# Performance work log

Hardware: AMD Instinct MI355X
Metric: run time of the kernel (lower is better)

The kernel has to match this reference:

```python
import jax, jax.numpy as jnp
import numpy as np

CUTOFF = 5.0
COULOMB_CONSTANT = 14.3996454784936  # eV * Angstrom / e^2
SQRT2 = 1.4142135623730951
N_NODES = 500000
N_EDGES = 16000000


def polynomial_cutoff(r, cutoff):
    ratio = r / cutoff
    f = 1.0 - 6.0 * ratio**5 + 15.0 * ratio**4 - 10.0 * ratio**3
    return jnp.where(r <= cutoff, f, 0.0)


def setup_inputs() -> dict:
    key = jax.random.key(0)
    k1, k2, k3, k4, k5 = jax.random.split(key, 5)
    charge = jax.random.normal(k1, (N_NODES,), dtype=jnp.float32)
    # sigma in (0.5, 1.5): positive Gaussian widths
    sigma = jax.random.uniform(k2, (N_NODES,), dtype=jnp.float32) + 0.5
    # bond_dist in (0.1, CUTOFF)
    bond_dist = jax.random.uniform(k3, (N_EDGES,), dtype=jnp.float32) * (CUTOFF - 0.1) + 0.1
    src = jax.random.randint(k4, (N_EDGES,), 0, N_NODES, dtype=jnp.int32)
    dst = jax.random.randint(k5, (N_EDGES,), 0, N_NODES, dtype=jnp.int32)
    return {"charge": charge, "sigma": sigma, "bond_dist": bond_dist, "src": src, "dst": dst}


def reference(charge, sigma, bond_dist, src, dst):
    # Edge-wise message: q_dst * erf(r / (sqrt2 * gamma)) * fcut(r) / r * K
    gamma = jnp.sqrt(sigma[src] ** 2 + sigma[dst] ** 2)  # [E]
    msg = (
        charge[dst]
        * jax.scipy.special.erf(bond_dist / (SQRT2 * gamma))
        * polynomial_cutoff(bond_dist, CUTOFF)
        / bond_dist
    ) * COULOMB_CONSTANT
    # Sum-aggregate messages at destination nodes (DGL fn.sum semantics)
    elec_pot = jax.ops.segment_sum(msg, dst, num_segments=charge.shape[0])
    return elec_pot
```

## Files before the change

### kernel.cpp

```cpp
#include <hip/hip_runtime.h>
#include <hip/hip_fp16.h>
#include <math.h>
#include <stdint.h>

#define CUTOFF_F     5.0f
#define INV_CUTOFF   0.2f
#define KCOUL        14.3996454784936f
#define INV_SQRT2    0.7071067811865475f

typedef int            vint4    __attribute__((ext_vector_type(4)));
typedef float          vfloat4  __attribute__((ext_vector_type(4)));
typedef uint32_t       vuint4   __attribute__((ext_vector_type(4)));
typedef unsigned short vushort8 __attribute__((ext_vector_type(8)));

#define WSHIFT        12
#define WINDOW        4096
#define NB            123
#define WGS_PER_B     8
#define NWG2          (NB * WGS_PER_B)
#define EPT           8
#define EPB           4096
#define OFFS_STRIDE   128
#define SPAN_MAX      512

__device__ __forceinline__ float erf_approx(float x) {
    const float a1 = 0.254829592f, a2 = -0.284496736f, a3 = 1.421413741f,
                a4 = -1.453152027f, a5 = 1.061405429f, p = 0.3275911f;
    float t = __builtin_amdgcn_rcpf(fmaf(p, x, 1.0f));
    float poly = t * fmaf(t, fmaf(t, fmaf(t, fmaf(t, a5, a4), a3), a2), a1);
    return 1.0f - poly * __expf(-x * x);
}

__device__ __forceinline__ float edge_val(float rr, float s2sum) {
    float inv_gamma = rsqrtf(s2sum);
    float x  = rr * INV_CUTOFF;
    float fc = fmaf(x * x * x, fmaf(x, fmaf(-6.0f, x, 15.0f), -10.0f), 1.0f);
    fc = (rr <= CUTOFF_F) ? fc : 0.0f;
    return erf_approx(rr * INV_SQRT2 * inv_gamma) * fc * KCOUL
         * __builtin_amdgcn_rcpf(rr);
}

__global__ __launch_bounds__(256, 6) void p1_bin(
    const float* __restrict__ bond,
    const int*   __restrict__ src,
    const int*   __restrict__ dst,
    unsigned short* __restrict__ offs,
    uint32_t*       __restrict__ sl_out,
    unsigned short* __restrict__ r_out,
    int n_edges)
{
    __shared__ uint32_t hist[NB];
    __shared__ uint32_t scan_s[NB + 1];
    __shared__ alignas(16) uint32_t       buf_sl[EPB];
    __shared__ alignas(16) unsigned short buf_r[EPB];

    const int tid = threadIdx.x;
    const int e0  = blockIdx.x * EPB;

    if (tid < NB) hist[tid] = 0;
    __syncthreads();

    int   dA[EPT], sA[EPT], dB[EPT], sB[EPT];
    float rA[EPT], rB[EPT];
    const bool full = (e0 + EPB <= n_edges);
    if (full) {
        const vint4*   dp = (const vint4*)(dst + e0) + tid;
        const vint4*   sp = (const vint4*)(src + e0) + tid;
        const vfloat4* rp = (const vfloat4*)(bond + e0) + tid;
        vint4 d0 = __builtin_nontemporal_load(dp);
        vint4 d1 = __builtin_nontemporal_load(dp + 256);
        vint4 s0 = __builtin_nontemporal_load(sp);
        vint4 s1 = __builtin_nontemporal_load(sp + 256);
        vfloat4 r0 = __builtin_nontemporal_load(rp);
        vfloat4 r1 = __builtin_nontemporal_load(rp + 256);
        vint4 d2 = __builtin_nontemporal_load(dp + 512);
        vint4 d3 = __builtin_nontemporal_load(dp + 768);
        vint4 s2 = __builtin_nontemporal_load(sp + 512);
        vint4 s3 = __builtin_nontemporal_load(sp + 768);
        vfloat4 r2 = __builtin_nontemporal_load(rp + 512);
        vfloat4 r3 = __builtin_nontemporal_load(rp + 768);
        dA[0]=d0.x; dA[1]=d0.y; dA[2]=d0.z; dA[3]=d0.w;
        dA[4]=d1.x; dA[5]=d1.y; dA[6]=d1.z; dA[7]=d1.w;
        sA[0]=s0.x; sA[1]=s0.y; sA[2]=s0.z; sA[3]=s0.w;
        sA[4]=s1.x; sA[5]=s1.y; sA[6]=s1.z; sA[7]=s1.w;
        rA[0]=r0.x; rA[1]=r0.y; rA[2]=r0.z; rA[3]=r0.w;
        rA[4]=r1.x; rA[5]=r1.y; rA[6]=r1.z; rA[7]=r1.w;
        dB[0]=d2.x; dB[1]=d2.y; dB[2]=d2.z; dB[3]=d2.w;
        dB[4]=d3.x; dB[5]=d3.y; dB[6]=d3.z; dB[7]=d3.w;
        sB[0]=s2.x; sB[1]=s2.y; sB[2]=s2.z; sB[3]=s2.w;
        sB[4]=s3.x; sB[5]=s3.y; sB[6]=s3.z; sB[7]=s3.w;
        rB[0]=r2.x; rB[1]=r2.y; rB[2]=r2.z; rB[3]=r2.w;
        rB[4]=r3.x; rB[5]=r3.y; rB[6]=r3.z; rB[7]=r3.w;
    } else {
        #pragma unroll
        for (int j = 0; j < EPT; ++j) {
            int eA = e0 + (j >> 2) * 1024 + tid * 4 + (j & 3);
            int eB = eA + 2048;
            if (eA < n_edges) { dA[j] = dst[eA]; sA[j] = src[eA]; rA[j] = bond[eA]; }
            else dA[j] = -1;
            if (eB < n_edges) { dB[j] = dst[eB]; sB[j] = src[eB]; rB[j] = bond[eB]; }
            else dB[j] = -1;
        }
    }

    uint32_t slA[EPT], brA[EPT], slB[EPT], brB[EPT];
    unsigned short hrA[EPT], hrB[EPT];
    #pragma unroll
    for (int j = 0; j < EPT; ++j) {
        if (dA[j] >= 0) {
            unsigned b = (unsigned)dA[j] >> WSHIFT;
            uint32_t r = atomicAdd(&hist[b], 1u);
            brA[j] = (b << 16) | r;
            slA[j] = ((uint32_t)sA[j] << WSHIFT) | ((unsigned)dA[j] & (WINDOW - 1));
            hrA[j] = __half_as_ushort(__float2half_rn(rA[j]));
        } else brA[j] = 0xFFFFFFFFu;
    }
    #pragma unroll
    for (int j = 0; j < EPT; ++j) {
        if (dB[j] >= 0) {
            unsigned b = (unsigned)dB[j] >> WSHIFT;
            uint32_t r = atomicAdd(&hist[b], 1u);
            brB[j] = (b << 16) | r;
            slB[j] = ((uint32_t)sB[j] << WSHIFT) | ((unsigned)dB[j] & (WINDOW - 1));
            hrB[j] = __half_as_ushort(__float2half_rn(rB[j]));
        } else brB[j] = 0xFFFFFFFFu;
    }
    __syncthreads();

    if (tid < 64) {
        int i0 = 2 * tid, i1 = 2 * tid + 1;
        uint32_t v0 = (i0 < NB) ? hist[i0] : 0u;
        uint32_t v1 = (i1 < NB) ? hist[i1] : 0u;
        uint32_t s  = v0 + v1;
        uint32_t inc = s;
        #pragma unroll
        for (int d = 1; d < 64; d <<= 1) {
            uint32_t up = __shfl_up(inc, d, 64);
            if (tid >= d) inc += up;
        }
        uint32_t excl = inc - s;
        if (i0 < NB) scan_s[i0] = excl;
        if (i1 < NB) scan_s[i1] = excl + v0;
        if (tid == 63) scan_s[NB] = inc;
    }
    __syncthreads();

    #pragma unroll
    for (int j = 0; j < EPT; ++j)
        if (brA[j] != 0xFFFFFFFFu) {
            uint32_t p = scan_s[brA[j] >> 16] + (brA[j] & 0xFFFFu);
            buf_sl[p] = slA[j]; buf_r[p] = hrA[j];
        }
    #pragma unroll
    for (int j = 0; j < EPT; ++j)
        if (brB[j] != 0xFFFFFFFFu) {
            uint32_t p = scan_s[brB[j] >> 16] + (brB[j] & 0xFFFFu);
            buf_sl[p] = slB[j]; buf_r[p] = hrB[j];
        }
    __syncthreads();

    if (tid <= NB)
        offs[(size_t)blockIdx.x * OFFS_STRIDE + tid] = (unsigned short)scan_s[tid];

    {
        const vuint4* bs = (const vuint4*)buf_sl;
        vuint4* os = (vuint4*)(sl_out + (size_t)blockIdx.x * EPB);
        #pragma unroll
        for (int i = 0; i < EPB / 4 / 256; ++i)
            __builtin_nontemporal_store(bs[tid + i * 256], os + tid + i * 256);
        const vushort8* br = (const vushort8*)buf_r;
        vushort8* orr = (vushort8*)(r_out + (size_t)blockIdx.x * EPB);
        #pragma unroll
        for (int i = 0; i < EPB / 8 / 256; ++i)
            __builtin_nontemporal_store(br[tid + i * 256], orr + tid + i * 256);
    }
}

__global__ __launch_bounds__(256) void p2_acc(
    const uint32_t*       __restrict__ sl_in,
    const unsigned short* __restrict__ r_in,
    const unsigned short* __restrict__ offs,
    const float*          __restrict__ sigma,
    float*                __restrict__ partials,
    int n_nodes, int nblk)
{
    __shared__ float acc[WINDOW];
    __shared__ float sig[WINDOW];
    __shared__ unsigned short offLo[SPAN_MAX];
    __shared__ unsigned short offHi[SPAN_MAX];

    const int g = blockIdx.x;
    const int b = g / WGS_PER_B;
    const int w = g % WGS_PER_B;

    vfloat4* accv = (vfloat4*)acc;
    for (int i = threadIdx.x; i < WINDOW / 4; i += 256)
        accv[i] = (vfloat4){0.f, 0.f, 0.f, 0.f};

    const int nbase  = b << WSHIFT;
    const int nvalid = (n_nodes - nbase < WINDOW) ? (n_nodes - nbase) : WINDOW;
    if (nvalid == WINDOW) {
        vfloat4* sv = (vfloat4*)sig;
        const vfloat4* gp = (const vfloat4*)(sigma + nbase);
        for (int i = threadIdx.x; i < WINDOW / 4; i += 256) sv[i] = gp[i];
    } else {
        for (int i = threadIdx.x; i < WINDOW; i += 256)
            sig[i] = (i < nvalid) ? sigma[nbase + i] : 0.f;
    }

    const int span = (nblk + WGS_PER_B - 1) / WGS_PER_B;
    const int blk0 = w * span;
    int blkN = nblk - blk0;
    if (blkN > span) blkN = span;
    if (blkN < 0) blkN = 0;
    for (int i = threadIdx.x; i < blkN; i += 256) {
        size_t o = (size_t)(blk0 + i) * OFFS_STRIDE + b;
        offLo[i] = offs[o];
        offHi[i] = offs[o + 1];
    }
    __syncthreads();

    const int wave = threadIdx.x >> 6, lane = threadIdx.x & 63;
    for (int i = wave; i < blkN; i += 4) {
        uint32_t lo  = offLo[i];
        uint32_t len = (uint32_t)offHi[i] - lo;
        const uint32_t*       slb = sl_in + (size_t)(blk0 + i) * EPB + lo;
        const unsigned short* rb  = r_in  + (size_t)(blk0 + i) * EPB + lo;
        for (uint32_t k = lane; k < len; k += 64) {
            uint32_t sl = slb[k];
            float rr = __half2float(__ushort_as_half(rb[k]));
            float ss = sigma[sl >> WSHIFT];
            float sd = sig[sl & (WINDOW - 1)];
            float v  = edge_val(rr, fmaf(ss, ss, sd * sd));
            atomicAdd(&acc[sl & (WINDOW - 1)], v);
        }
    }
    __syncthreads();

    vfloat4* outp = (vfloat4*)(partials + (size_t)g * WINDOW);
    for (int i = threadIdx.x; i < WINDOW / 4; i += 256)
        __builtin_nontemporal_store(accv[i], outp + i);
}

__global__ __launch_bounds__(256) void p3_reduce(
    const float* __restrict__ partials,
    const float* __restrict__ charge,
    float*       __restrict__ out, int n_nodes)
{
    int n = blockIdx.x * 256 + threadIdx.x;
    if (n >= n_nodes) return;
    unsigned b     = (unsigned)n >> WSHIFT;
    unsigned local = (unsigned)n & (WINDOW - 1);
    const float* p = partials + ((size_t)b * WGS_PER_B) * WINDOW + local;
    float sum = 0.0f;
    #pragma unroll
    for (int w = 0; w < WGS_PER_B; ++w)
        sum += __builtin_nontemporal_load(p + (size_t)w * WINDOW);
    out[n] = charge[n] * sum;
}

__global__ __launch_bounds__(256) void edge_msg_atomic(
    const float* __restrict__ charge, const float* __restrict__ sigma,
    const float* __restrict__ bond, const int* __restrict__ src,
    const int* __restrict__ dst, float* __restrict__ out, int n_edges)
{
    int i = blockIdx.x * blockDim.x + threadIdx.x;
    if (i < n_edges) {
        float ss = sigma[src[i]], sd = sigma[dst[i]];
        float msg = charge[dst[i]] * edge_val(bond[i], fmaf(ss, ss, sd * sd));
        atomicAdd(&out[dst[i]], msg);
    }
}

extern "C" void kernel_launch(void* const* d_in, const int* in_sizes, int n_in,
                              void* d_out, int out_size, void* d_ws, size_t ws_size,
                              hipStream_t stream) {
    const float* charge = (const float*)d_in[0];
    const float* sigma  = (const float*)d_in[1];
    const float* bond   = (const float*)d_in[2];
    const int*   src    = (const int*)d_in[3];
    const int*   dst    = (const int*)d_in[4];
    float* out = (float*)d_out;

    int n_nodes = in_sizes[0];
    int n_edges = in_sizes[2];

    int nblk = (n_edges + EPB - 1) / EPB;
    int span = (nblk + WGS_PER_B - 1) / WGS_PER_B;

    size_t offs_b = (size_t)nblk * OFFS_STRIDE * sizeof(unsigned short);
    size_t sl_b   = (size_t)nblk * EPB * sizeof(uint32_t);
    size_t r_b    = (size_t)nblk * EPB * sizeof(unsigned short);
    size_t part_b = (size_t)NWG2 * WINDOW * sizeof(float);
    size_t need   = offs_b + sl_b + r_b + part_b;

    if (n_nodes <= NB * WINDOW && need <= ws_size && span <= SPAN_MAX) {
        unsigned short* offs = (unsigned short*)d_ws;
        uint32_t*       slp  = (uint32_t*)((char*)d_ws + offs_b);
        unsigned short* rp   = (unsigned short*)((char*)d_ws + offs_b + sl_b);
        float* partial = (float*)((char*)d_ws + offs_b + sl_b + r_b);

        p1_bin<<<nblk, 256, 0, stream>>>(bond, src, dst, offs, slp, rp, n_edges);
        p2_acc<<<NWG2, 256, 0, stream>>>(slp, rp, offs, sigma, partial,
                                         n_nodes, nblk);
        int blocks3 = (n_nodes + 255) / 256;
        p3_reduce<<<blocks3, 256, 0, stream>>>(partial, charge, out, n_nodes);
    } else {
        (void)hipMemsetAsync(out, 0, (size_t)n_nodes * sizeof(float), stream);
        int blocks = (n_edges + 255) / 256;
        edge_msg_atomic<<<blocks, 256, 0, stream>>>(charge, sigma, bond, src, dst,
                                                    out, n_edges);
    }
}
```

Before: 346.2 us.

## Flatten per-block segments via prefix scan for balanced wave work in p2_acc

Replaces the per-source-block wave loop, where each wave processed one short segment with partially idle lanes, with a flattened edge index space. A wave-level scan builds cumulative segment lengths, each wave takes an equal contiguous chunk, and lanes locate their segment by binary search plus a linear walk. The intent is to remove lane underutilization on short segments (about 4096/123 ≈ 33 edges each) and to balance load across waves. The cost is an extra scan, a barrier and per-lane segment walks. A launch-bounds occupancy hint is also added.

```diff
diff --git a/kernel.cpp b/kernel.cpp
--- a/kernel.cpp
+++ b/kernel.cpp
@@ -176,7 +176,7 @@
     }
 }
 
-__global__ __launch_bounds__(256) void p2_acc(
+__global__ __launch_bounds__(256, 4) void p2_acc(
     const uint32_t*       __restrict__ sl_in,
     const unsigned short* __restrict__ r_in,
     const unsigned short* __restrict__ offs,
@@ -187,7 +187,7 @@
     __shared__ float acc[WINDOW];
     __shared__ float sig[WINDOW];
     __shared__ unsigned short offLo[SPAN_MAX];
-    __shared__ unsigned short offHi[SPAN_MAX];
+    __shared__ uint32_t cum[SPAN_MAX + 1];
 
     const int g = blockIdx.x;
     const int b = g / WGS_PER_B;
@@ -215,24 +215,61 @@
     if (blkN < 0) blkN = 0;
     for (int i = threadIdx.x; i < blkN; i += 256) {
         size_t o = (size_t)(blk0 + i) * OFFS_STRIDE + b;
-        offLo[i] = offs[o];
-        offHi[i] = offs[o + 1];
+        unsigned short lo = offs[o];
+        offLo[i] = lo;
+        cum[i] = (uint32_t)offs[o + 1] - lo;
+    }
+    __syncthreads();
+
+    if (threadIdx.x < 64) {
+        const int base = threadIdx.x * 8;
+        uint32_t v[8]; uint32_t s = 0;
+        #pragma unroll
+        for (int j = 0; j < 8; ++j) { v[j] = (base + j < blkN) ? cum[base + j] : 0u; s += v[j]; }
+        uint32_t inc = s;
+        #pragma unroll
+        for (int d = 1; d < 64; d <<= 1) {
+            uint32_t up = __shfl_up(inc, d, 64);
+            if (threadIdx.x >= d) inc += up;
+        }
+        uint32_t excl = inc - s;
+        #pragma unroll
+        for (int j = 0; j < 8; ++j) { uint32_t t = v[j]; cum[base + j] = excl; excl += t; }
+        if (threadIdx.x == 63) cum[SPAN_MAX] = inc;
     }
     __syncthreads();
 
     const int wave = threadIdx.x >> 6, lane = threadIdx.x & 63;
-    for (int i = wave; i < blkN; i += 4) {
-        uint32_t lo  = offLo[i];
-        uint32_t len = (uint32_t)offHi[i] - lo;
-        const uint32_t*       slb = sl_in + (size_t)(blk0 + i) * EPB + lo;
-        const unsigned short* rb  = r_in  + (size_t)(blk0 + i) * EPB + lo;
-        for (uint32_t k = lane; k < len; k += 64) {
-            uint32_t sl = slb[k];
-            float rr = __half2float(__ushort_as_half(rb[k]));
-            float ss = sigma[sl >> WSHIFT];
-            float sd = sig[sl & (WINDOW - 1)];
-            float v  = edge_val(rr, fmaf(ss, ss, sd * sd));
-            atomicAdd(&acc[sl & (WINDOW - 1)], v);
+    const uint32_t T = cum[blkN];
+
+    const uint32_t chunk = (T + 3) >> 2;
+    const uint32_t f0    = (uint32_t)wave * chunk;
+    uint32_t fend        = f0 + chunk;
+    if (fend > T) fend = T;
+
+    if (f0 < fend) {
+        int l = 0, r = blkN;
+        while (l < r) {
+            int m = (l + r) >> 1;
+            if (cum[m + 1] <= f0) l = m + 1; else r = m;
+        }
+        int i = l;
+
+        for (uint32_t fb = f0; fb < fend; fb += 64) {
+            uint32_t f = fb + lane;
+            int ii = i;
+            if (f < fend) {
+                while (cum[ii + 1] <= f) ++ii;
+                uint32_t k = f - cum[ii];
+                size_t addr = (size_t)(blk0 + ii) * EPB + offLo[ii] + k;
+                uint32_t sl = sl_in[addr];
+                float rr = __half2float(__ushort_as_half(r_in[addr]));
+                float ss = sigma[sl >> WSHIFT];
+                float sd = sig[sl & (WINDOW - 1)];
+                float v  = edge_val(rr, fmaf(ss, ss, sd * sd));
+                atomicAdd(&acc[sl & (WINDOW - 1)], v);
+            }
+            i = __shfl(ii, 63);
         }
     }
     __syncthreads();
```

Result: no change. 345.4 us (-0.2%).

## Bin edges into global per-window buckets via atomic reservation and halve window size

Applied to the files above, without the earlier changes.

The binning pass now reserves space in per-destination-window global buckets (fixed capacity CAP) with an atomic counter per bucket. It scatters each block's sorted edges directly into those buckets, so the accumulation pass reads one contiguous, vector-loadable range per window instead of walking per-block offset tables. The window shrinks to 2048 nodes with 245 buckets, and occupancy hints are retuned. The catch is that the binning writes become narrow scattered stores, and there is no per-bucket overflow check, so a skewed destination distribution that exceeds CAP in one bucket would corrupt results.

```diff
diff --git a/kernel.cpp b/kernel.cpp
--- a/kernel.cpp
+++ b/kernel.cpp
@@ -11,17 +11,16 @@
 typedef int            vint4    __attribute__((ext_vector_type(4)));
 typedef float          vfloat4  __attribute__((ext_vector_type(4)));
 typedef uint32_t       vuint4   __attribute__((ext_vector_type(4)));
-typedef unsigned short vushort8 __attribute__((ext_vector_type(8)));
-
-#define WSHIFT        12
-#define WINDOW        4096
-#define NB            123
+typedef unsigned short vushort4 __attribute__((ext_vector_type(4)));
+
+#define WSHIFT        11
+#define WINDOW        2048
+#define NB            245
 #define WGS_PER_B     8
 #define NWG2          (NB * WGS_PER_B)
 #define EPT           8
 #define EPB           4096
-#define OFFS_STRIDE   128
-#define SPAN_MAX      512
+#define CAP           71680
 
 __device__ __forceinline__ float erf_approx(float x) {
     const float a1 = 0.254829592f, a2 = -0.284496736f, a3 = 1.421413741f,
@@ -40,19 +39,21 @@
          * __builtin_amdgcn_rcpf(rr);
 }
 
-__global__ __launch_bounds__(256, 6) void p1_bin(
+__global__ __launch_bounds__(256, 4) void p1_bin(
     const float* __restrict__ bond,
     const int*   __restrict__ src,
     const int*   __restrict__ dst,
-    unsigned short* __restrict__ offs,
+    uint32_t*       __restrict__ ctr,
     uint32_t*       __restrict__ sl_out,
     unsigned short* __restrict__ r_out,
     int n_edges)
 {
     __shared__ uint32_t hist[NB];
     __shared__ uint32_t scan_s[NB + 1];
+    __shared__ uint32_t gbase[NB];
     __shared__ alignas(16) uint32_t       buf_sl[EPB];
     __shared__ alignas(16) unsigned short buf_r[EPB];
+    __shared__ uint8_t  bkt[EPB];
 
     const int tid = threadIdx.x;
     const int e0  = blockIdx.x * EPB;
@@ -128,10 +129,10 @@
     __syncthreads();
 
     if (tid < 64) {
-        int i0 = 2 * tid, i1 = 2 * tid + 1;
-        uint32_t v0 = (i0 < NB) ? hist[i0] : 0u;
-        uint32_t v1 = (i1 < NB) ? hist[i1] : 0u;
-        uint32_t s  = v0 + v1;
+        const int base = tid * 4;
+        uint32_t v[4]; uint32_t s = 0;
+        #pragma unroll
+        for (int j = 0; j < 4; ++j) { v[j] = (base + j < NB) ? hist[base + j] : 0u; s += v[j]; }
         uint32_t inc = s;
         #pragma unroll
         for (int d = 1; d < 64; d <<= 1) {
@@ -139,9 +140,11 @@
             if (tid >= d) inc += up;
         }
         uint32_t excl = inc - s;
-        if (i0 < NB) scan_s[i0] = excl;
-        if (i1 < NB) scan_s[i1] = excl + v0;
-        if (tid == 63) scan_s[NB] = inc;
+        #pragma unroll
+        for (int j = 0; j < 4; ++j) {
+            if (base + j <= NB) scan_s[base + j] = excl;
+            excl += v[j];
+        }
     }
     __syncthreads();
 
@@ -149,45 +152,45 @@
     for (int j = 0; j < EPT; ++j)
         if (brA[j] != 0xFFFFFFFFu) {
             uint32_t p = scan_s[brA[j] >> 16] + (brA[j] & 0xFFFFu);
-            buf_sl[p] = slA[j]; buf_r[p] = hrA[j];
+            buf_sl[p] = slA[j]; buf_r[p] = hrA[j]; bkt[p] = (uint8_t)(brA[j] >> 16);
         }
     #pragma unroll
     for (int j = 0; j < EPT; ++j)
         if (brB[j] != 0xFFFFFFFFu) {
             uint32_t p = scan_s[brB[j] >> 16] + (brB[j] & 0xFFFFu);
-            buf_sl[p] = slB[j]; buf_r[p] = hrB[j];
-        }
-    __syncthreads();
-
-    if (tid <= NB)
-        offs[(size_t)blockIdx.x * OFFS_STRIDE + tid] = (unsigned short)scan_s[tid];
-
-    {
-        const vuint4* bs = (const vuint4*)buf_sl;
-        vuint4* os = (vuint4*)(sl_out + (size_t)blockIdx.x * EPB);
-        #pragma unroll
-        for (int i = 0; i < EPB / 4 / 256; ++i)
-            __builtin_nontemporal_store(bs[tid + i * 256], os + tid + i * 256);
-        const vushort8* br = (const vushort8*)buf_r;
-        vushort8* orr = (vushort8*)(r_out + (size_t)blockIdx.x * EPB);
-        #pragma unroll
-        for (int i = 0; i < EPB / 8 / 256; ++i)
-            __builtin_nontemporal_store(br[tid + i * 256], orr + tid + i * 256);
-    }
-}
-
-__global__ __launch_bounds__(256) void p2_acc(
+            buf_sl[p] = slB[j]; buf_r[p] = hrB[j]; bkt[p] = (uint8_t)(brB[j] >> 16);
+        }
+
+    if (tid < NB) {
+        uint32_t len = scan_s[tid + 1] - scan_s[tid];
+        uint32_t base = atomicAdd(&ctr[tid], len);
+        gbase[tid] = (uint32_t)tid * CAP + base - scan_s[tid];
+    }
+    __syncthreads();
+
+    const int total = (int)scan_s[NB];
+    #pragma unroll
+    for (int i = 0; i < EPB / 256; ++i) {
+        int p = tid + i * 256;
+        if (p < total) {
+            unsigned bb = bkt[p];
+            uint32_t addr = gbase[bb] + (uint32_t)p;
+            __builtin_nontemporal_store(buf_sl[p], sl_out + addr);
+            __builtin_nontemporal_store(buf_r[p],  r_out + addr);
+        }
+    }
+}
+
+__global__ __launch_bounds__(256, 6) void p2_acc(
     const uint32_t*       __restrict__ sl_in,
     const unsigned short* __restrict__ r_in,
-    const unsigned short* __restrict__ offs,
+    const uint32_t*       __restrict__ ctr,
     const float*          __restrict__ sigma,
     float*                __restrict__ partials,
-    int n_nodes, int nblk)
+    int n_nodes)
 {
     __shared__ float acc[WINDOW];
     __shared__ float sig[WINDOW];
-    __shared__ unsigned short offLo[SPAN_MAX];
-    __shared__ unsigned short offHi[SPAN_MAX];
 
     const int g = blockIdx.x;
     const int b = g / WGS_PER_B;
@@ -207,32 +210,30 @@
         for (int i = threadIdx.x; i < WINDOW; i += 256)
             sig[i] = (i < nvalid) ? sigma[nbase + i] : 0.f;
     }
-
-    const int span = (nblk + WGS_PER_B - 1) / WGS_PER_B;
-    const int blk0 = w * span;
-    int blkN = nblk - blk0;
-    if (blkN > span) blkN = span;
-    if (blkN < 0) blkN = 0;
-    for (int i = threadIdx.x; i < blkN; i += 256) {
-        size_t o = (size_t)(blk0 + i) * OFFS_STRIDE + b;
-        offLo[i] = offs[o];
-        offHi[i] = offs[o + 1];
-    }
-    __syncthreads();
-
-    const int wave = threadIdx.x >> 6, lane = threadIdx.x & 63;
-    for (int i = wave; i < blkN; i += 4) {
-        uint32_t lo  = offLo[i];
-        uint32_t len = (uint32_t)offHi[i] - lo;
-        const uint32_t*       slb = sl_in + (size_t)(blk0 + i) * EPB + lo;
-        const unsigned short* rb  = r_in  + (size_t)(blk0 + i) * EPB + lo;
-        for (uint32_t k = lane; k < len; k += 64) {
-            uint32_t sl = slb[k];
-            float rr = __half2float(__ushort_as_half(rb[k]));
-            float ss = sigma[sl >> WSHIFT];
-            float sd = sig[sl & (WINDOW - 1)];
-            float v  = edge_val(rr, fmaf(ss, ss, sd * sd));
-            atomicAdd(&acc[sl & (WINDOW - 1)], v);
+    __syncthreads();
+
+    const uint32_t cnt   = ctr[b];
+    uint32_t chunk = (((cnt + WGS_PER_B - 1) / WGS_PER_B) + 3u) & ~3u;
+    const uint32_t start = (uint32_t)w * chunk;
+    uint32_t end = start + chunk;
+    if (end > cnt) end = cnt;
+
+    const uint32_t*       slb = sl_in + (size_t)b * CAP;
+    const unsigned short* rb  = r_in  + (size_t)b * CAP;
+
+    for (uint32_t r0 = start + (uint32_t)threadIdx.x * 4u; r0 < end; r0 += 1024u) {
+        vuint4   sl4 = *(const vuint4*)(slb + r0);
+        vushort4 r4  = *(const vushort4*)(rb + r0);
+        #pragma unroll
+        for (int j = 0; j < 4; ++j) {
+            if (r0 + (uint32_t)j < end) {
+                uint32_t sl = sl4[j];
+                float rr = __half2float(__ushort_as_half(r4[j]));
+                float ss = sigma[sl >> WSHIFT];
+                float sd = sig[sl & (WINDOW - 1)];
+                float v  = edge_val(rr, fmaf(ss, ss, sd * sd));
+                atomicAdd(&acc[sl & (WINDOW - 1)], v);
+            }
         }
     }
     __syncthreads();
@@ -286,23 +287,25 @@
     int n_edges = in_sizes[2];
 
     int nblk = (n_edges + EPB - 1) / EPB;
-    int span = (nblk + WGS_PER_B - 1) / WGS_PER_B;
-
-    size_t offs_b = (size_t)nblk * OFFS_STRIDE * sizeof(unsigned short);
-    size_t sl_b   = (size_t)nblk * EPB * sizeof(uint32_t);
-    size_t r_b    = (size_t)nblk * EPB * sizeof(unsigned short);
+
+    size_t ctr_b  = 1024;
+    size_t sl_b   = (size_t)NB * CAP * sizeof(uint32_t);
+    size_t r_b    = (size_t)NB * CAP * sizeof(unsigned short);
     size_t part_b = (size_t)NWG2 * WINDOW * sizeof(float);
-    size_t need   = offs_b + sl_b + r_b + part_b;
-
-    if (n_nodes <= NB * WINDOW && need <= ws_size && span <= SPAN_MAX) {
-        unsigned short* offs = (unsigned short*)d_ws;
-        uint32_t*       slp  = (uint32_t*)((char*)d_ws + offs_b);
-        unsigned short* rp   = (unsigned short*)((char*)d_ws + offs_b + sl_b);
-        float* partial = (float*)((char*)d_ws + offs_b + sl_b + r_b);
-
-        p1_bin<<<nblk, 256, 0, stream>>>(bond, src, dst, offs, slp, rp, n_edges);
-        p2_acc<<<NWG2, 256, 0, stream>>>(slp, rp, offs, sigma, partial,
-                                         n_nodes, nblk);
+    size_t need   = ctr_b + sl_b + r_b + part_b;
+
+    bool cap_ok = ((size_t)n_edges <= (size_t)NB * CAP);
+
+    if (n_nodes <= NB * WINDOW && need <= ws_size && cap_ok &&
+        n_edges >= (1 << 20)) {
+        uint32_t*       ctrp = (uint32_t*)d_ws;
+        uint32_t*       slp  = (uint32_t*)((char*)d_ws + ctr_b);
+        unsigned short* rp   = (unsigned short*)((char*)d_ws + ctr_b + sl_b);
+        float* partial = (float*)((char*)d_ws + ctr_b + sl_b + r_b);
+
+        (void)hipMemsetAsync(ctrp, 0, NB * sizeof(uint32_t), stream);
+        p1_bin<<<nblk, 256, 0, stream>>>(bond, src, dst, ctrp, slp, rp, n_edges);
+        p2_acc<<<NWG2, 256, 0, stream>>>(slp, rp, ctrp, sigma, partial, n_nodes);
         int blocks3 = (n_nodes + 255) / 256;
         p3_reduce<<<blocks3, 256, 0, stream>>>(partial, charge, out, n_nodes);
     } else {
```

Result: slower. 410.7 us (+18.6%).
